# Performance work log

Measured on AMD Instinct MI355X. Metric: run time of the kernel, lower is better.

The kernel has to match this reference:

```python
import jax, jax.numpy as jnp
import numpy as np

NUM_HEADS = 16
NEG_INF = -1e30  # finite large negative; avoids NaN on fully-masked padded query rows


def setup_inputs() -> dict:
    key = jax.random.key(0)
    k0, k1, k2, k3 = jax.random.split(key, 4)
    B, S, E = 4, 2048, 1024
    x_padded = jax.random.normal(k0, (B, S, E), dtype=jnp.float32)
    # variable lengths in [S//2, S] so no batch row is fully empty
    seq_lengths = jax.random.randint(k1, (B,), S // 2, S + 1).astype(jnp.int32)
    Wqkv = jax.random.normal(k2, (3 * E, E), dtype=jnp.float32) * 0.02  # torch Linear weight [out,in]
    Wout = jax.random.normal(k3, (E, E), dtype=jnp.float32) * 0.02
    return {"x_padded": x_padded, "Wqkv": Wqkv, "Wout": Wout,
            "seq_lengths": seq_lengths, "window_left": 512, "window_right": 0}


def _build_mask(seq_lengths, S, window_left, window_right):
    # key-side padding mask: [B, S]
    pad = jnp.arange(S)[None, :] < seq_lengths[:, None]
    mask = pad[:, None, None, :]  # [B,1,1,S]
    if window_left >= 0 or window_right >= 0:
        i = jnp.arange(S)[:, None]
        j = jnp.arange(S)[None, :]
        win = jnp.ones((S, S), dtype=bool)
        if window_left >= 0:
            win = win & (j >= i - window_left)
        if window_right >= 0:
            win = win & (j <= i + window_right)
        mask = mask & win[None, None, :, :]
    elif (window_left, window_right) == (-1, 0):
        causal = jnp.tril(jnp.ones((S, S), dtype=bool))
        mask = mask & causal[None, None, :, :]
    return mask  # [B,1,S,S] (broadcasts over heads)


def reference(x_padded, Wqkv, Wout, seq_lengths, window_left, window_right):
    B, S, E = x_padded.shape
    H = NUM_HEADS
    D = E // H
    scale = 1.0 / jnp.sqrt(jnp.float32(D))
    qkv = x_padded @ Wqkv.T  # [B,S,3E]
    q, k, v = jnp.split(qkv, 3, axis=-1)
    q = q.reshape(B, S, H, D).transpose(0, 2, 1, 3)  # [B,H,S,D]
    k = k.reshape(B, S, H, D).transpose(0, 2, 1, 3)
    v = v.reshape(B, S, H, D).transpose(0, 2, 1, 3)
    mask = _build_mask(seq_lengths, S, window_left, window_right)
    scores = jnp.einsum("bhid,bhjd->bhij", q, k) * scale
    scores = jnp.where(mask, scores, NEG_INF)
    attn = jax.nn.softmax(scores, axis=-1)
    out = jnp.einsum("bhij,bhjd->bhid", attn, v)  # [B,H,S,D]
    out = out.transpose(0, 2, 1, 3).reshape(B, S, E)
    return out @ Wout.T
```

## Files before the change

### kernel.cpp

```cpp
#include <hip/hip_runtime.h>

typedef __bf16 bf16;
typedef __attribute__((ext_vector_type(2))) __bf16 bf16x2;
typedef __attribute__((ext_vector_type(4))) __bf16 bf16x4;
typedef __attribute__((ext_vector_type(8))) __bf16 bf16x8;
typedef __attribute__((ext_vector_type(4))) float f32x4;
typedef __attribute__((ext_vector_type(16))) float f32x16;

#define B_ 4
#define S_ 2048
#define H_ 16
#define D_ 64
#define E_ 1024

#define BM 256
#define BN 128
#define BK 64

__device__ __forceinline__ int imin(int a, int b) { return a < b ? a : b; }
__device__ __forceinline__ int imax(int a, int b) { return a > b ? a : b; }

__device__ __forceinline__ void gload_lds16(const void* g, void* l) {
  __builtin_amdgcn_global_load_lds(
      (const __attribute__((address_space(1))) void*)g,
      (__attribute__((address_space(3))) void*)l, 16, 0, 0);
}

__global__ __launch_bounds__(256) void f32_to_bf16_kernel(
    const float* __restrict__ in, bf16* __restrict__ out, int n) {
  int i = (blockIdx.x * 256 + threadIdx.x) * 8;
  const int stride = gridDim.x * 256 * 8;
  for (; i < n; i += stride) {
    float4 v0 = *(const float4*)(in + i);
    float4 v1 = *(const float4*)(in + i + 4);
    bf16x8 o;
    o[0] = (bf16)v0.x; o[1] = (bf16)v0.y; o[2] = (bf16)v0.z; o[3] = (bf16)v0.w;
    o[4] = (bf16)v1.x; o[5] = (bf16)v1.y; o[6] = (bf16)v1.z; o[7] = (bf16)v1.w;
    *(bf16x8*)(out + i) = o;
  }
}

__global__ __launch_bounds__(512, 1) void gemm_pipe(
    const bf16* __restrict__ A, const bf16* __restrict__ Bm,
    int M, int N, int K, int mode,
    bf16* __restrict__ qd, bf16* __restrict__ kd, bf16* __restrict__ vtd,
    float* __restrict__ outf) {
  __shared__ __align__(16) bf16 As[3][BM * BK];
  __shared__ __align__(16) bf16 Bs[3][BN * BK];
  const int tid = threadIdx.x;
  const int wave = tid >> 6, lane = tid & 63;
  const int l15 = lane & 15, l4 = lane >> 4;
  const int wm = (wave >> 1) * 64;
  const int wn = (wave & 1) * 64;

  const int nwg = gridDim.x * gridDim.y;
  const int fid = blockIdx.y * gridDim.x + blockIdx.x;
  const int chunk = nwg >> 3;
  const int swz = (fid & 7) * chunk + (fid >> 3);
  const int tn = swz % gridDim.x;
  const int tm = swz / gridDim.x;

  const bf16* Abase = A + (size_t)tm * BM * K;
  const bf16* Bbase = Bm + (size_t)tn * BN * K;

  f32x4 acc[4][4];
#pragma unroll
  for (int i = 0; i < 4; ++i)
#pragma unroll
    for (int j = 0; j < 4; ++j)
#pragma unroll
      for (int r = 0; r < 4; ++r) acc[i][j][r] = 0.f;

  const int NT = K >> 6;

#define STAGE_A(sbuf, k0)                                                      \
  {                                                                            \
    _Pragma("unroll") for (int ld = 0; ld < 4; ++ld) {                         \
      const int idx = ld * 512 + tid;                                          \
      const int row = idx >> 3, g = idx & 7;                                   \
      const int gs = g ^ (((row >> 2) & 1) << 1);                              \
      gload_lds16(Abase + (size_t)row * K + (k0) + gs * 8,                     \
                  As[sbuf] + (ld * 512 + wave * 64) * 8);                      \
    }                                                                          \
  }
#define STAGE_B(sbuf, k0)                                                      \
  {                                                                            \
    _Pragma("unroll") for (int ld = 0; ld < 2; ++ld) {                         \
      const int idx = ld * 512 + tid;                                          \
      const int row = idx >> 3, g = idx & 7;                                   \
      const int gs = g ^ (((row >> 2) & 1) << 1);                              \
      gload_lds16(Bbase + (size_t)row * K + (k0) + gs * 8,                     \
                  Bs[sbuf] + (ld * 512 + wave * 64) * 8);                      \
    }                                                                          \
  }

  STAGE_A(0, 0); STAGE_B(0, 0);
  STAGE_A(1, BK); STAGE_B(1, BK);
  asm volatile("s_waitcnt vmcnt(6)" ::: "memory");
  __builtin_amdgcn_s_barrier();

  int p = 0;
  for (int t = 0; t < NT; ++t) {
    const bf16* Ap = As[p];
    const bf16* Bp = Bs[p];
    const int sb = (p + 2 >= 3) ? p - 1 : p + 2;
    const int sk0 = ((t + 2 < NT) ? t + 2 : NT - 1) * BK;

    bf16x8 a[4], bfr[4];
#pragma unroll
    for (int i = 0; i < 4; ++i) {
      const int ra = wm + i * 16 + l15;
      a[i] = *(const bf16x8*)(Ap + ra * 64 + ((l4 * 8) ^ (((ra >> 2) & 1) << 4)));
      const int rb = wn + i * 16 + l15;
      bfr[i] = *(const bf16x8*)(Bp + rb * 64 + ((l4 * 8) ^ (((rb >> 2) & 1) << 4)));
    }
    STAGE_A(sb, sk0);
    __builtin_amdgcn_s_setprio(1);
#pragma unroll
    for (int i = 0; i < 4; ++i)
#pragma unroll
      for (int j = 0; j < 4; ++j)
        acc[i][j] = __builtin_amdgcn_mfma_f32_16x16x32_bf16(a[i], bfr[j],
                                                            acc[i][j], 0, 0, 0);
    __builtin_amdgcn_s_setprio(0);
#pragma unroll
    for (int i = 0; i < 4; ++i) {
      const int ra = wm + i * 16 + l15;
      a[i] = *(const bf16x8*)(Ap + ra * 64 + ((32 + l4 * 8) ^ (((ra >> 2) & 1) << 4)));
      const int rb = wn + i * 16 + l15;
      bfr[i] = *(const bf16x8*)(Bp + rb * 64 + ((32 + l4 * 8) ^ (((rb >> 2) & 1) << 4)));
    }
    STAGE_B(sb, sk0);
    __builtin_amdgcn_s_setprio(1);
#pragma unroll
    for (int i = 0; i < 4; ++i)
#pragma unroll
      for (int j = 0; j < 4; ++j)
        acc[i][j] = __builtin_amdgcn_mfma_f32_16x16x32_bf16(a[i], bfr[j],
                                                            acc[i][j], 0, 0, 0);
    __builtin_amdgcn_s_setprio(0);

    asm volatile("s_waitcnt vmcnt(6)" ::: "memory");
    __builtin_amdgcn_s_barrier();
    p = (p + 1 >= 3) ? 0 : p + 1;
  }
#undef STAGE_A
#undef STAGE_B

  if (mode == 0) {
#pragma unroll
    for (int i = 0; i < 4; ++i) {
      const int m0 = tm * BM + wm + i * 16 + l4 * 4;
      const int b = m0 >> 11, s = m0 & (S_ - 1);
#pragma unroll
      for (int j = 0; j < 4; ++j) {
        const int n = tn * BN + wn + j * 16 + l15;
        const int which = n >> 10;
        const int hn = n & 1023;
        const int h = hn >> 6, d = hn & 63;
        const f32x4 av = acc[i][j];
        if (which == 0) {
#pragma unroll
          for (int r = 0; r < 4; ++r)
            qd[((size_t)(b * H_ + h) * S_ + (s + r)) * D_ + d] =
                (bf16)(av[r] * 0.125f);
        } else if (which == 1) {
#pragma unroll
          for (int r = 0; r < 4; ++r)
            kd[((size_t)(b * H_ + h) * S_ + (s + r)) * D_ + d] = (bf16)av[r];
        } else {
          bf16x4 pv;
#pragma unroll
          for (int r = 0; r < 4; ++r) pv[r] = (bf16)av[r];
          *(bf16x4*)(vtd + ((size_t)(b * H_ + h) * D_ + d) * S_ + s) = pv;
        }
      }
    }
  } else {
#pragma unroll
    for (int i = 0; i < 4; ++i) {
      const int m0 = tm * BM + wm + i * 16 + l4 * 4;
#pragma unroll
      for (int j = 0; j < 4; ++j) {
        const int n = tn * BN + wn + j * 16 + l15;
#pragma unroll
        for (int r = 0; r < 4; ++r) outf[(size_t)(m0 + r) * N + n] = acc[i][j][r];
      }
    }
  }
}

__global__ __launch_bounds__(256) void meanv_kernel(const bf16* __restrict__ vt,
                                                    float* __restrict__ meanv) {
  __shared__ float part[256];
  const int bh = blockIdx.x;
  const int tid = threadIdx.x;
  const int d = tid & 63, seg = tid >> 6;
  const bf16* row = vt + ((size_t)bh * D_ + d) * S_ + seg * 512;
  float s = 0.f;
  for (int i = 0; i < 512; i += 8) {
    bf16x8 v = *(const bf16x8*)(row + i);
#pragma unroll
    for (int j = 0; j < 8; ++j) s += (float)v[j];
  }
  part[tid] = s;
  __syncthreads();
  if (tid < 64) {
    float t = part[tid] + part[64 + tid] + part[128 + tid] + part[192 + tid];
    meanv[(size_t)bh * D_ + tid] = t * (1.0f / (float)S_);
  }
}

__device__ __forceinline__ int pk2(float a, float b) {
  union { bf16x2 h; int i; } u;
  u.h[0] = (bf16)a; u.h[1] = (bf16)b;
  return u.i;
}

__global__ __launch_bounds__(128) void attn_kernel(
    const bf16* __restrict__ q, const bf16* __restrict__ k,
    const bf16* __restrict__ vt, const float* __restrict__ meanv,
    const int* __restrict__ seq_lengths, const int* __restrict__ wlp,
    const int* __restrict__ wrp, bf16* __restrict__ attn_out) {
  __shared__ float Lm[64], Ll[64];
  __shared__ float Lo[32][64];
  const int tid = threadIdx.x, wave = tid >> 6, lane = tid & 63;
  const int l31 = lane & 31, l5 = lane >> 5;
  const int bid0 = blockIdx.x;
  const int bid = (bid0 & 7) * 512 + (bid0 >> 3);
  const int bh = bid >> 6;
  const int g = bid & 63;
  const int b = bh >> 4, h = bh & 15;
  const int q0w = g * 32;
  const int seq_len = seq_lengths[b];
  const int wl = wlp[0], wr = wrp[0];

  const bf16* qbase = q + (size_t)bh * S_ * D_;
  const bf16* kbase = k + (size_t)bh * S_ * D_;
  const bf16* vtb = vt + (size_t)bh * D_ * S_;

  bf16x8 qa[4];
#pragma unroll
  for (int dg = 0; dg < 4; ++dg)
    qa[dg] = *(const bf16x8*)(qbase + (size_t)(q0w + l31) * D_ + dg * 16 + l5 * 8);

  const int hi_ = (wr >= 0) ? imin(q0w + 31 + wr, S_ - 1) : (S_ - 1);
  const int kv_end = imin(hi_ + 1, seq_len);
  const int lo_ = (wl >= 0) ? imax(0, q0w - wl) : 0;
  const int kv_begin = lo_ & ~31;
  const int span = kv_end - kv_begin;
  const int nt = (span > 0) ? ((span + 31) >> 5) : 0;

  f32x16 o0, o1;
#pragma unroll
  for (int r = 0; r < 16; ++r) { o0[r] = 0.f; o1[r] = 0.f; }
  float mrun = -1e30f, lrun = 0.f;

  int kt0 = kv_begin + wave * 32;
  if (wave >= nt) kt0 = kv_begin;
  bf16x8 kreg[4];
#pragma unroll
  for (int dg = 0; dg < 4; ++dg)
    kreg[dg] = *(const bf16x8*)(kbase + (size_t)(kt0 + l31) * D_ + dg * 16 + l5 * 8);

  for (int t = wave; t < nt; t += 2) {
    const int kt = kv_begin + t * 32;
    f32x16 sf;
#pragma unroll
    for (int r = 0; r < 16; ++r) sf[r] = 0.f;
#pragma unroll
    for (int dg = 0; dg < 4; ++dg)
      sf = __builtin_amdgcn_mfma_f32_32x32x16_bf16(kreg[dg], qa[dg], sf, 0, 0, 0);

    bf16x8 vreg[4];
#pragma unroll
    for (int kg = 0; kg < 2; ++kg) {
      vreg[kg * 2 + 0] = *(const bf16x8*)(vtb + (size_t)(l31) * S_ + kt + kg * 16 + l5 * 8);
      vreg[kg * 2 + 1] = *(const bf16x8*)(vtb + (size_t)(32 + l31) * S_ + kt + kg * 16 + l5 * 8);
    }
    int ktn = kv_begin + (t + 2) * 32;
    if (t + 2 >= nt) ktn = kv_begin;
#pragma unroll
    for (int dg = 0; dg < 4; ++dg)
      kreg[dg] = *(const bf16x8*)(kbase + (size_t)(ktn + l31) * D_ + dg * 16 + l5 * 8);

    bool allv = (kt + 31 < seq_len);
    if (wr >= 0) allv = allv && (kt + 31 <= q0w + wr);
    if (wl >= 0) allv = allv && (kt >= q0w + 31 - wl);

    float p[16];
    float tmax = -1e30f;
    if (allv) {
#pragma unroll
      for (int r = 0; r < 16; ++r) { p[r] = sf[r]; tmax = fmaxf(tmax, p[r]); }
    } else {
      const int qrow = q0w + l31;
#pragma unroll
      for (int r = 0; r < 16; ++r) {
        const int key = kt + (r & 3) + 8 * (r >> 2) + 4 * l5;
        bool valid = (key < seq_len);
        if (wr >= 0) valid = valid && (key <= qrow + wr);
        if (wl >= 0) valid = valid && (key >= qrow - wl);
        p[r] = valid ? sf[r] : -1e30f;
        tmax = fmaxf(tmax, p[r]);
      }
    }
    tmax = fmaxf(tmax, __shfl_xor(tmax, 32, 64));

    if (!__all(tmax <= mrun + 8.0f)) {
      const float mnew = fmaxf(mrun, tmax);
      const float corr = __expf(mrun - mnew);
      mrun = mnew;
      lrun *= corr;
#pragma unroll
      for (int r = 0; r < 16; ++r) { o0[r] *= corr; o1[r] *= corr; }
    }

    float lsum = 0.f;
#pragma unroll
    for (int r = 0; r < 16; ++r) {
      const float pe = (p[r] <= -1e29f) ? 0.f : __expf(p[r] - mrun);
      p[r] = pe;
      lsum += pe;
    }
    lsum += __shfl_xor(lsum, 32, 64);
    lrun += lsum;

    bf16x8 pb[2];
#pragma unroll
    for (int kg = 0; kg < 2; ++kg) {
      const int w0 = pk2(p[kg * 8 + 0], p[kg * 8 + 1]);
      const int w1 = pk2(p[kg * 8 + 2], p[kg * 8 + 3]);
      const int w2 = pk2(p[kg * 8 + 4], p[kg * 8 + 5]);
      const int w3 = pk2(p[kg * 8 + 6], p[kg * 8 + 7]);
      auto r02 = __builtin_amdgcn_permlane32_swap(w0, w2, false, false);
      auto r13 = __builtin_amdgcn_permlane32_swap(w1, w3, false, false);
      union { int i[4]; bf16x8 v; } u;
      u.i[0] = r02[0]; u.i[1] = r13[0]; u.i[2] = r02[1]; u.i[3] = r13[1];
      pb[kg] = u.v;
    }

#pragma unroll
    for (int kg = 0; kg < 2; ++kg) {
      o0 = __builtin_amdgcn_mfma_f32_32x32x16_bf16(vreg[kg * 2 + 0], pb[kg], o0, 0, 0, 0);
      o1 = __builtin_amdgcn_mfma_f32_32x32x16_bf16(vreg[kg * 2 + 1], pb[kg], o1, 0, 0, 0);
    }
  }

  if (wave == 1) {
    Lm[lane] = mrun;
    Ll[lane] = lrun;
#pragma unroll
    for (int r = 0; r < 16; ++r) {
      Lo[r][lane] = o0[r];
      Lo[16 + r][lane] = o1[r];
    }
  }
  __syncthreads();
  if (wave == 1) return;

  const float m2 = Lm[lane], l2 = Ll[lane];
  const float ms = fmaxf(mrun, m2);
  const float w1 = __expf(mrun - ms), w2 = __expf(m2 - ms);
  const float ls = lrun * w1 + l2 * w2;
#pragma unroll
  for (int r = 0; r < 16; ++r) {
    o0[r] = o0[r] * w1 + Lo[r][lane] * w2;
    o1[r] = o1[r] * w1 + Lo[16 + r][lane] * w2;
  }

  const int qrow = q0w + l31;
  bf16* outp = attn_out + ((size_t)(b * S_ + qrow)) * E_ + h * 64;
  if (ls > 0.f) {
    const float inv = 1.0f / ls;
#pragma unroll
    for (int dg2 = 0; dg2 < 2; ++dg2) {
      const f32x16& o = dg2 ? o1 : o0;
#pragma unroll
      for (int rg = 0; rg < 4; ++rg) {
        const int d0 = dg2 * 32 + 8 * rg + 4 * l5;
        bf16x4 ov;
#pragma unroll
        for (int j = 0; j < 4; ++j) ov[j] = (bf16)(o[rg * 4 + j] * inv);
        *(bf16x4*)(outp + d0) = ov;
      }
    }
  } else {
    const float* mv = meanv + (size_t)bh * D_;
#pragma unroll
    for (int dg2 = 0; dg2 < 2; ++dg2)
#pragma unroll
      for (int rg = 0; rg < 4; ++rg) {
        const int d0 = dg2 * 32 + 8 * rg + 4 * l5;
        bf16x4 ov;
#pragma unroll
        for (int j = 0; j < 4; ++j) ov[j] = (bf16)mv[d0 + j];
        *(bf16x4*)(outp + d0) = ov;
      }
  }
}

extern "C" void kernel_launch(void* const* d_in, const int* in_sizes, int n_in,
                              void* d_out, int out_size, void* d_ws, size_t ws_size,
                              hipStream_t stream) {
  const float* x = (const float*)d_in[0];
  const float* Wqkv = (const float*)d_in[1];
  const float* Wout = (const float*)d_in[2];
  const int* seq_lengths = (const int*)d_in[3];
  const int* wl = (const int*)d_in[4];
  const int* wr = (const int*)d_in[5];
  float* out = (float*)d_out;

  char* ws = (char*)d_ws;
  bf16* xb = (bf16*)ws;      ws += (size_t)8192 * 1024 * 2;
  bf16* wqkvb = (bf16*)ws;   ws += (size_t)3072 * 1024 * 2;
  bf16* woutb = (bf16*)ws;   ws += (size_t)1024 * 1024 * 2;
  bf16* qd = (bf16*)ws;      ws += (size_t)B_ * H_ * S_ * D_ * 2;
  bf16* kd = (bf16*)ws;      ws += (size_t)B_ * H_ * S_ * D_ * 2;
  bf16* vtd = (bf16*)ws;     ws += (size_t)B_ * H_ * S_ * D_ * 2;
  bf16* attn = (bf16*)ws;    ws += (size_t)8192 * 1024 * 2;
  float* meanv = (float*)ws; ws += (size_t)B_ * H_ * D_ * 4;

  f32_to_bf16_kernel<<<2048, 256, 0, stream>>>(x, xb, 8192 * 1024);
  f32_to_bf16_kernel<<<768, 256, 0, stream>>>(Wqkv, wqkvb, 3072 * 1024);
  f32_to_bf16_kernel<<<512, 256, 0, stream>>>(Wout, woutb, 1024 * 1024);

  gemm_pipe<<<dim3(24, 32), 512, 0, stream>>>(xb, wqkvb, 8192, 3072, 1024, 0,
                                              qd, kd, vtd, nullptr);
  meanv_kernel<<<64, 256, 0, stream>>>(vtd, meanv);
  attn_kernel<<<4096, 128, 0, stream>>>(qd, kd, vtd, meanv, seq_lengths, wl, wr,
                                        attn);
  gemm_pipe<<<dim3(8, 32), 512, 0, stream>>>(attn, woutb, 8192, 1024, 1024, 1,
                                             nullptr, nullptr, nullptr, out);
}
```

Before: 187.7 us.

## Share K/V tiles in LDS across four query waves per block

Restructures the attention kernel so each 256-thread block handles 128 query rows with four waves, one per 32-row slice. K and V are staged into double-buffered, XOR-swizzled LDS 64-key tiles with async global-to-LDS loads, so all four waves reuse each tile. Before, each wave loaded K/V straight from global memory and two waves split the key range, then merged results. The change removes that split-KV merge and cuts redundant global traffic, but it adds a barrier per tile and makes waves idle on tiles outside their own window.

```diff
diff --git a/kernel.cpp b/kernel.cpp
--- a/kernel.cpp
+++ b/kernel.cpp
@@ -217,21 +217,22 @@
   return u.i;
 }
 
-__global__ __launch_bounds__(128) void attn_kernel(
+__global__ __launch_bounds__(256) void attn_kernel(
     const bf16* __restrict__ q, const bf16* __restrict__ k,
     const bf16* __restrict__ vt, const float* __restrict__ meanv,
     const int* __restrict__ seq_lengths, const int* __restrict__ wlp,
     const int* __restrict__ wrp, bf16* __restrict__ attn_out) {
-  __shared__ float Lm[64], Ll[64];
-  __shared__ float Lo[32][64];
+  __shared__ __align__(16) bf16 Ks[2][64 * 64];
+  __shared__ __align__(16) bf16 Vs[2][64 * 64];
   const int tid = threadIdx.x, wave = tid >> 6, lane = tid & 63;
   const int l31 = lane & 31, l5 = lane >> 5;
   const int bid0 = blockIdx.x;
-  const int bid = (bid0 & 7) * 512 + (bid0 >> 3);
-  const int bh = bid >> 6;
-  const int g = bid & 63;
+  const int bid = (bid0 & 7) * 128 + (bid0 >> 3);
+  const int bh = bid >> 4;
+  const int g = bid & 15;
   const int b = bh >> 4, h = bh & 15;
-  const int q0w = g * 32;
+  const int q0b = g * 128;
+  const int q0w = q0b + wave * 32;
   const int seq_len = seq_lengths[b];
   const int wl = wlp[0], wr = wrp[0];
 
@@ -244,135 +245,149 @@
   for (int dg = 0; dg < 4; ++dg)
     qa[dg] = *(const bf16x8*)(qbase + (size_t)(q0w + l31) * D_ + dg * 16 + l5 * 8);
 
-  const int hi_ = (wr >= 0) ? imin(q0w + 31 + wr, S_ - 1) : (S_ - 1);
-  const int kv_end = imin(hi_ + 1, seq_len);
-  const int lo_ = (wl >= 0) ? imax(0, q0w - wl) : 0;
-  const int kv_begin = lo_ & ~31;
-  const int span = kv_end - kv_begin;
-  const int nt = (span > 0) ? ((span + 31) >> 5) : 0;
+  const int hi_blk = (wr >= 0) ? imin(q0b + 127 + wr, S_ - 1) : (S_ - 1);
+  const int end_blk = imin(hi_blk + 1, seq_len);
+  const int lo_blk = (wl >= 0) ? imax(0, q0b - wl) : 0;
+  const int beg_blk = lo_blk & ~63;
+  const int ntb = (end_blk > beg_blk) ? ((end_blk - beg_blk + 63) >> 6) : 0;
+
+  const int w_hi = (wr >= 0) ? (q0w + 31 + wr) : (S_ - 1);
+  const int w_end = imin(w_hi + 1, seq_len);
+  const int w_lo = (wl >= 0) ? imax(0, q0w - wl) : 0;
 
   f32x16 o0, o1;
 #pragma unroll
   for (int r = 0; r < 16; ++r) { o0[r] = 0.f; o1[r] = 0.f; }
   float mrun = -1e30f, lrun = 0.f;
 
-  int kt0 = kv_begin + wave * 32;
-  if (wave >= nt) kt0 = kv_begin;
-  bf16x8 kreg[4];
-#pragma unroll
-  for (int dg = 0; dg < 4; ++dg)
-    kreg[dg] = *(const bf16x8*)(kbase + (size_t)(kt0 + l31) * D_ + dg * 16 + l5 * 8);
-
-  for (int t = wave; t < nt; t += 2) {
-    const int kt = kv_begin + t * 32;
-    f32x16 sf;
-#pragma unroll
-    for (int r = 0; r < 16; ++r) sf[r] = 0.f;
-#pragma unroll
-    for (int dg = 0; dg < 4; ++dg)
-      sf = __builtin_amdgcn_mfma_f32_32x32x16_bf16(kreg[dg], qa[dg], sf, 0, 0, 0);
-
-    bf16x8 vreg[4];
-#pragma unroll
-    for (int kg = 0; kg < 2; ++kg) {
-      vreg[kg * 2 + 0] = *(const bf16x8*)(vtb + (size_t)(l31) * S_ + kt + kg * 16 + l5 * 8);
-      vreg[kg * 2 + 1] = *(const bf16x8*)(vtb + (size_t)(32 + l31) * S_ + kt + kg * 16 + l5 * 8);
-    }
-    int ktn = kv_begin + (t + 2) * 32;
-    if (t + 2 >= nt) ktn = kv_begin;
-#pragma unroll
-    for (int dg = 0; dg < 4; ++dg)
-      kreg[dg] = *(const bf16x8*)(kbase + (size_t)(ktn + l31) * D_ + dg * 16 + l5 * 8);
-
-    bool allv = (kt + 31 < seq_len);
-    if (wr >= 0) allv = allv && (kt + 31 <= q0w + wr);
-    if (wl >= 0) allv = allv && (kt >= q0w + 31 - wl);
-
-    float p[16];
-    float tmax = -1e30f;
-    if (allv) {
-#pragma unroll
-      for (int r = 0; r < 16; ++r) { p[r] = sf[r]; tmax = fmaxf(tmax, p[r]); }
-    } else {
-      const int qrow = q0w + l31;
+#define STAGE(bufb, kt0)                                                       \
+  {                                                                            \
+    _Pragma("unroll") for (int ld = 0; ld < 2; ++ld) {                         \
+      const int idx = ld * 256 + tid;                                          \
+      const int row = idx >> 3, gg = idx & 7;                                  \
+      const int gs = gg ^ (row & 7);                                           \
+      const int krow = imin((kt0) + row, S_ - 1);                              \
+      gload_lds16(kbase + (size_t)krow * 64 + gs * 8, Ks[bufb] + idx * 8);     \
+      const int vcol = imin((kt0) + gs * 8, S_ - 8);                           \
+      gload_lds16(vtb + (size_t)row * S_ + vcol, Vs[bufb] + idx * 8);          \
+    }                                                                          \
+  }
+#define LDS_K(bufb, row, gran)                                                 \
+  (*(const bf16x8*)((const char*)(Ks[bufb]) + (row) * 128 +                    \
+                    (((gran) ^ ((row) & 7)) << 4)))
+#define LDS_V(bufb, row, gran)                                                 \
+  (*(const bf16x8*)((const char*)(Vs[bufb]) + (row) * 128 +                    \
+                    (((gran) ^ ((row) & 7)) << 4)))
+
+  if (ntb > 0) STAGE(0, beg_blk);
+  __syncthreads();
+
+  for (int t = 0; t < ntb; ++t) {
+    const int kt = beg_blk + t * 64;
+    if (t + 1 < ntb) STAGE((t + 1) & 1, kt + 64);
+
+    const bool active = (kt < w_end) && (kt + 63 >= w_lo);
+    if (active) {
+      const int bufb = t & 1;
+      f32x16 sf0, sf1;
+#pragma unroll
+      for (int r = 0; r < 16; ++r) { sf0[r] = 0.f; sf1[r] = 0.f; }
+#pragma unroll
+      for (int dg = 0; dg < 4; ++dg) {
+        bf16x8 kb0 = LDS_K(bufb, l31, dg * 2 + l5);
+        bf16x8 kb1 = LDS_K(bufb, 32 + l31, dg * 2 + l5);
+        sf0 = __builtin_amdgcn_mfma_f32_32x32x16_bf16(kb0, qa[dg], sf0, 0, 0, 0);
+        sf1 = __builtin_amdgcn_mfma_f32_32x32x16_bf16(kb1, qa[dg], sf1, 0, 0, 0);
+      }
+
+      bool allv = (kt + 63 < seq_len);
+      if (wr >= 0) allv = allv && (kt + 63 <= q0w + wr);
+      if (wl >= 0) allv = allv && (kt >= q0w + 31 - wl);
+      if (!allv) {
+        const int qrow = q0w + l31;
+#pragma unroll
+        for (int hh = 0; hh < 2; ++hh)
+#pragma unroll
+          for (int r = 0; r < 16; ++r) {
+            const int key = kt + hh * 32 + (r & 3) + 8 * (r >> 2) + 4 * l5;
+            bool valid = (key < seq_len);
+            if (wr >= 0) valid = valid && (key <= qrow + wr);
+            if (wl >= 0) valid = valid && (key >= qrow - wl);
+            if (hh == 0) sf0[r] = valid ? sf0[r] : -1e30f;
+            else sf1[r] = valid ? sf1[r] : -1e30f;
+          }
+      }
+      float tmax = -1e30f;
 #pragma unroll
       for (int r = 0; r < 16; ++r) {
-        const int key = kt + (r & 3) + 8 * (r >> 2) + 4 * l5;
-        bool valid = (key < seq_len);
-        if (wr >= 0) valid = valid && (key <= qrow + wr);
-        if (wl >= 0) valid = valid && (key >= qrow - wl);
-        p[r] = valid ? sf[r] : -1e30f;
-        tmax = fmaxf(tmax, p[r]);
-      }
-    }
-    tmax = fmaxf(tmax, __shfl_xor(tmax, 32, 64));
-
-    if (!__all(tmax <= mrun + 8.0f)) {
-      const float mnew = fmaxf(mrun, tmax);
-      const float corr = __expf(mrun - mnew);
-      mrun = mnew;
-      lrun *= corr;
-#pragma unroll
-      for (int r = 0; r < 16; ++r) { o0[r] *= corr; o1[r] *= corr; }
-    }
-
-    float lsum = 0.f;
-#pragma unroll
-    for (int r = 0; r < 16; ++r) {
-      const float pe = (p[r] <= -1e29f) ? 0.f : __expf(p[r] - mrun);
-      p[r] = pe;
-      lsum += pe;
-    }
-    lsum += __shfl_xor(lsum, 32, 64);
-    lrun += lsum;
-
-    bf16x8 pb[2];
-#pragma unroll
-    for (int kg = 0; kg < 2; ++kg) {
-      const int w0 = pk2(p[kg * 8 + 0], p[kg * 8 + 1]);
-      const int w1 = pk2(p[kg * 8 + 2], p[kg * 8 + 3]);
-      const int w2 = pk2(p[kg * 8 + 4], p[kg * 8 + 5]);
-      const int w3 = pk2(p[kg * 8 + 6], p[kg * 8 + 7]);
-      auto r02 = __builtin_amdgcn_permlane32_swap(w0, w2, false, false);
-      auto r13 = __builtin_amdgcn_permlane32_swap(w1, w3, false, false);
-      union { int i[4]; bf16x8 v; } u;
-      u.i[0] = r02[0]; u.i[1] = r13[0]; u.i[2] = r02[1]; u.i[3] = r13[1];
-      pb[kg] = u.v;
-    }
-
-#pragma unroll
-    for (int kg = 0; kg < 2; ++kg) {
-      o0 = __builtin_amdgcn_mfma_f32_32x32x16_bf16(vreg[kg * 2 + 0], pb[kg], o0, 0, 0, 0);
-      o1 = __builtin_amdgcn_mfma_f32_32x32x16_bf16(vreg[kg * 2 + 1], pb[kg], o1, 0, 0, 0);
-    }
-  }
-
-  if (wave == 1) {
-    Lm[lane] = mrun;
-    Ll[lane] = lrun;
-#pragma unroll
-    for (int r = 0; r < 16; ++r) {
-      Lo[r][lane] = o0[r];
-      Lo[16 + r][lane] = o1[r];
-    }
-  }
-  __syncthreads();
-  if (wave == 1) return;
-
-  const float m2 = Lm[lane], l2 = Ll[lane];
-  const float ms = fmaxf(mrun, m2);
-  const float w1 = __expf(mrun - ms), w2 = __expf(m2 - ms);
-  const float ls = lrun * w1 + l2 * w2;
-#pragma unroll
-  for (int r = 0; r < 16; ++r) {
-    o0[r] = o0[r] * w1 + Lo[r][lane] * w2;
-    o1[r] = o1[r] * w1 + Lo[16 + r][lane] * w2;
-  }
+        tmax = fmaxf(tmax, sf0[r]);
+        tmax = fmaxf(tmax, sf1[r]);
+      }
+      tmax = fmaxf(tmax, __shfl_xor(tmax, 32, 64));
+
+      if (!__all(tmax <= mrun + 8.0f)) {
+        const float mnew = fmaxf(mrun, tmax);
+        const float corr = __expf(mrun - mnew);
+        mrun = mnew;
+        lrun *= corr;
+#pragma unroll
+        for (int r = 0; r < 16; ++r) { o0[r] *= corr; o1[r] *= corr; }
+      }
+
+      float lsum = 0.f;
+#pragma unroll
+      for (int r = 0; r < 16; ++r) {
+        const float e0 = (sf0[r] <= -1e29f) ? 0.f : __expf(sf0[r] - mrun);
+        const float e1 = (sf1[r] <= -1e29f) ? 0.f : __expf(sf1[r] - mrun);
+        sf0[r] = e0; sf1[r] = e1;
+        lsum += e0 + e1;
+      }
+      lsum += __shfl_xor(lsum, 32, 64);
+      lrun += lsum;
+
+      bf16x8 pb[4];
+#pragma unroll
+      for (int kg = 0; kg < 4; ++kg) {
+        const int base = (kg & 1) * 8;
+        float p0, p1, p2, p3, p4, p5, p6, p7;
+        if (kg < 2) {
+          p0 = sf0[base + 0]; p1 = sf0[base + 1]; p2 = sf0[base + 2];
+          p3 = sf0[base + 3]; p4 = sf0[base + 4]; p5 = sf0[base + 5];
+          p6 = sf0[base + 6]; p7 = sf0[base + 7];
+        } else {
+          p0 = sf1[base + 0]; p1 = sf1[base + 1]; p2 = sf1[base + 2];
+          p3 = sf1[base + 3]; p4 = sf1[base + 4]; p5 = sf1[base + 5];
+          p6 = sf1[base + 6]; p7 = sf1[base + 7];
+        }
+        const int w0 = pk2(p0, p1);
+        const int w1 = pk2(p2, p3);
+        const int w2 = pk2(p4, p5);
+        const int w3 = pk2(p6, p7);
+        auto r02 = __builtin_amdgcn_permlane32_swap(w0, w2, false, false);
+        auto r13 = __builtin_amdgcn_permlane32_swap(w1, w3, false, false);
+        union { int i[4]; bf16x8 v; } u;
+        u.i[0] = r02[0]; u.i[1] = r13[0]; u.i[2] = r02[1]; u.i[3] = r13[1];
+        pb[kg] = u.v;
+      }
+
+#pragma unroll
+      for (int kg = 0; kg < 4; ++kg) {
+        bf16x8 va0 = LDS_V(bufb, l31, kg * 2 + l5);
+        bf16x8 va1 = LDS_V(bufb, 32 + l31, kg * 2 + l5);
+        o0 = __builtin_amdgcn_mfma_f32_32x32x16_bf16(va0, pb[kg], o0, 0, 0, 0);
+        o1 = __builtin_amdgcn_mfma_f32_32x32x16_bf16(va1, pb[kg], o1, 0, 0, 0);
+      }
+    }
+    __syncthreads();
+  }
+#undef STAGE
+#undef LDS_K
+#undef LDS_V
 
   const int qrow = q0w + l31;
   bf16* outp = attn_out + ((size_t)(b * S_ + qrow)) * E_ + h * 64;
-  if (ls > 0.f) {
-    const float inv = 1.0f / ls;
+  if (lrun > 0.f) {
+    const float inv = 1.0f / lrun;
 #pragma unroll
     for (int dg2 = 0; dg2 < 2; ++dg2) {
       const f32x16& o = dg2 ? o1 : o0;
@@ -428,7 +443,7 @@
   gemm_pipe<<<dim3(24, 32), 512, 0, stream>>>(xb, wqkvb, 8192, 3072, 1024, 0,
                                               qd, kd, vtd, nullptr);
   meanv_kernel<<<64, 256, 0, stream>>>(vtd, meanv);
-  attn_kernel<<<4096, 128, 0, stream>>>(qd, kd, vtd, meanv, seq_lengths, wl, wr,
+  attn_kernel<<<1024, 256, 0, stream>>>(qd, kd, vtd, meanv, seq_lengths, wl, wr,
                                         attn);
   gemm_pipe<<<dim3(8, 32), 512, 0, stream>>>(attn, woutb, 8192, 1024, 1024, 1,
                                              nullptr, nullptr, nullptr, out);
```

Result: faster. 177.3 us (-5.5%).
